# Kernel optimization log

Measured on AMD Instinct MI355X. Metric: run time of the kernel, lower is better.

## Reference

```python
import jax, jax.numpy as jnp
import numpy as np

B, S, D = 2, 2048, 1024
H, HKV, HD = 16, 4, 64
FF = 4096
WINDOW = 1024
EPS = 1e-6


def _rope_tables(seq_len, head_dim, base=10000.0):
    inv_freq = 1.0 / (base ** (np.arange(0, head_dim, 2, dtype=np.float32) / head_dim))
    t = np.arange(seq_len, dtype=np.float32)
    freqs = np.outer(t, inv_freq)                       # [S, HD/2]
    emb = np.concatenate([freqs, freqs], axis=-1)       # [S, HD]
    return jnp.asarray(np.cos(emb)), jnp.asarray(np.sin(emb))


def setup_inputs() -> dict:
    key = jax.random.key(0)
    ks = jax.random.split(key, 16)
    s = lambda fan: 1.0 / np.sqrt(fan)
    cos, sin = _rope_tables(S, HD)
    return {
        "hidden_states": jax.random.normal(ks[0], (B, S, D), jnp.float32),
        "cos": cos, "sin": sin,
        "wq": jax.random.normal(ks[1], (D, H * HD), jnp.float32) * s(D),
        "bq": jnp.zeros((H * HD,), jnp.float32),
        "wk": jax.random.normal(ks[2], (D, HKV * HD), jnp.float32) * s(D),
        "bk": jnp.zeros((HKV * HD,), jnp.float32),
        "wv": jax.random.normal(ks[3], (D, HKV * HD), jnp.float32) * s(D),
        "bv": jnp.zeros((HKV * HD,), jnp.float32),
        "wo": jax.random.normal(ks[4], (H * HD, D), jnp.float32) * s(H * HD),
        "ln1_w": jnp.ones((D,), jnp.float32),
        "ln2_w": jnp.ones((D,), jnp.float32),
        "w_gate": jax.random.normal(ks[5], (D, FF), jnp.float32) * s(D),
        "w_up": jax.random.normal(ks[6], (D, FF), jnp.float32) * s(D),
        "w_down": jax.random.normal(ks[7], (FF, D), jnp.float32) * s(FF),
    }


def _rmsnorm(x, w, eps=EPS):
    var = jnp.mean(x.astype(jnp.float32) ** 2, axis=-1, keepdims=True)
    return (x * jax.lax.rsqrt(var + eps)).astype(x.dtype) * w


def _rotate_half(x):
    x1, x2 = jnp.split(x, 2, axis=-1)
    return jnp.concatenate([-x2, x1], axis=-1)


def reference(hidden_states, cos, sin, wq, bq, wk, bk, wv, bv, wo,
              ln1_w, ln2_w, w_gate, w_up, w_down):
    residual = hidden_states
    h = _rmsnorm(hidden_states, ln1_w)

    # projections -> [B, S, H, HD]
    q = (h @ wq + bq).reshape(B, S, H, HD)
    k = (h @ wk + bk).reshape(B, S, HKV, HD)
    v = (h @ wv + bv).reshape(B, S, HKV, HD)

    # RoPE
    c = cos[None, :, None, :]
    sn = sin[None, :, None, :]
    q = q * c + _rotate_half(q) * sn
    k = k * c + _rotate_half(k) * sn

    # GQA: repeat KV heads to H heads
    groups = H // HKV
    k = jnp.repeat(k, groups, axis=2)  # [B, S, H, HD]
    v = jnp.repeat(v, groups, axis=2)

    # sliding-window causal attention (flex_attention block-mask semantics)
    scale = 1.0 / np.sqrt(HD)
    scores = jnp.einsum("bqhd,bkhd->bhqk", q, k) * scale  # [B, H, S, S]
    i = jnp.arange(S)[:, None]
    j = jnp.arange(S)[None, :]
    mask = (j <= i) & (i - j < WINDOW)
    scores = jnp.where(mask[None, None], scores, jnp.finfo(scores.dtype).min)
    attn = jax.nn.softmax(scores, axis=-1)
    ctx = jnp.einsum("bhqk,bkhd->bqhd", attn, v).reshape(B, S, H * HD)

    h = residual + ctx @ wo

    residual2 = h
    h2 = _rmsnorm(h, ln2_w)
    mlp = (jax.nn.silu(h2 @ w_gate) * (h2 @ w_up)) @ w_down
    return residual2 + mlp
```

## Files before the change

kernel.cpp:

```cpp
#include <hip/hip_runtime.h>
#include <hip/hip_bf16.h>
#include <hip/hip_fp16.h>
#include <math.h>

#define BB 2
#define SS 2048
#define DD 1024
#define HH 16
#define HKVN 4
#define HDIM 64
#define FFD 4096
#define WND 1024
#define EPSF 1e-6f

typedef _Float16 f16;
typedef _Float16 half8 __attribute__((ext_vector_type(8)));
typedef float f32x4 __attribute__((ext_vector_type(4)));
typedef unsigned int u32;

#define GLOAD_LDS(gp, lp)                                                  \
  __builtin_amdgcn_global_load_lds(                                        \
      (const __attribute__((address_space(1))) u32*)(gp),                  \
      (__attribute__((address_space(3))) u32*)(lp), 16, 0, 0)

static __device__ inline u32 pack2(float a, float b) {
  unsigned short ua = __builtin_bit_cast(unsigned short, (f16)a);
  unsigned short ub = __builtin_bit_cast(unsigned short, (f16)b);
  return (u32)ua | ((u32)ub << 16);
}

__global__ __launch_bounds__(256) void prep_weights_kernel(
    const float* __restrict__ wq, const float* __restrict__ wk,
    const float* __restrict__ wv, const float* __restrict__ wo,
    const float* __restrict__ wg, const float* __restrict__ wu,
    const float* __restrict__ wd, const float* __restrict__ bq,
    const float* __restrict__ bk, const float* __restrict__ bv,
    f16* __restrict__ qkvT, f16* __restrict__ woT, f16* __restrict__ wgT,
    f16* __restrict__ wuT, f16* __restrict__ wdT, float* __restrict__ biasC) {
  int t = blockIdx.x;
  if (t >= 3712) {
    int i = (t - 3712) * 256 + threadIdx.x;
    if (i < 1024)
      biasC[i] = bq[i];
    else if (i < 1280)
      biasC[i] = bk[i - 1024];
    else if (i < 1536)
      biasC[i] = bv[i - 1280];
    return;
  }
  const float* W;
  f16* Wt;
  int K, N, lt;
  if (t < 256) {
    W = wq; Wt = qkvT; K = 1024; N = 1024; lt = t;
  } else if (t < 320) {
    W = wk; Wt = qkvT + (size_t)1024 * 1024; K = 1024; N = 256; lt = t - 256;
  } else if (t < 384) {
    W = wv; Wt = qkvT + (size_t)1280 * 1024; K = 1024; N = 256; lt = t - 320;
  } else if (t < 640) {
    W = wo; Wt = woT; K = 1024; N = 1024; lt = t - 384;
  } else if (t < 1664) {
    W = wg; Wt = wgT; K = 1024; N = 4096; lt = t - 640;
  } else if (t < 2688) {
    W = wu; Wt = wuT; K = 1024; N = 4096; lt = t - 1664;
  } else {
    W = wd; Wt = wdT; K = 4096; N = 1024; lt = t - 2688;
  }
  int ntx = N >> 6;
  int n0 = (lt % ntx) * 64, k0 = (lt / ntx) * 64;
  __shared__ float tile[64][65];
  int tx = threadIdx.x & 63, tr = threadIdx.x >> 6;
#pragma unroll
  for (int i = 0; i < 16; i++) {
    int r = tr + i * 4;
    tile[r][tx] = W[(size_t)(k0 + r) * N + n0 + tx];
  }
  __syncthreads();
#pragma unroll
  for (int i = 0; i < 16; i++) {
    int r = tr + i * 4;
    Wt[(size_t)(n0 + r) * K + k0 + tx] = (f16)tile[tx][r];
  }
}

__global__ __launch_bounds__(256) void rmsnorm_kernel(
    const float* __restrict__ x, const float* __restrict__ w,
    f16* __restrict__ out) {
  int row = blockIdx.x;
  int tid = threadIdx.x;
  float4 v = ((const float4*)(x + (size_t)row * 1024))[tid];
  float ss = v.x * v.x + v.y * v.y + v.z * v.z + v.w * v.w;
  for (int o = 32; o > 0; o >>= 1) ss += __shfl_down(ss, o, 64);
  __shared__ float red[4];
  int wid = tid >> 6, lane = tid & 63;
  if (lane == 0) red[wid] = ss;
  __syncthreads();
  if (tid == 0)
    red[0] = rsqrtf((red[0] + red[1] + red[2] + red[3]) / 1024.f + EPSF);
  __syncthreads();
  float rs = red[0];
  float4 wv = ((const float4*)w)[tid];
  u32 lo = pack2(v.x * rs * wv.x, v.y * rs * wv.y);
  u32 hi = pack2(v.z * rs * wv.z, v.w * rs * wv.w);
  *(int2*)(out + (size_t)row * 1024 + tid * 4) = make_int2((int)lo, (int)hi);
}

__global__ __launch_bounds__(256) void mfma_gemm(
    const f16* __restrict__ A, const f16* __restrict__ Bt,
    const float* __restrict__ bias, const float* __restrict__ resid,
    float* __restrict__ Cf, float* __restrict__ Cf2, f16* __restrict__ Ch,
    int M, int N, int K, int KL) {
  __shared__ __align__(16) char smem[3 * 16384];
  const int tid = threadIdx.x;
  const int lane = tid & 63;
  const int wid = tid >> 6;
  const int wr = wid >> 1, wc = wid & 1;
  const int row0 = blockIdx.y * 128, col0 = blockIdx.x * 128;
  const int koff = blockIdx.z * KL;

  f32x4 acc[4][4];
#pragma unroll
  for (int m = 0; m < 4; m++)
#pragma unroll
    for (int n = 0; n < 4; n++) acc[m][n] = (f32x4){0.f, 0.f, 0.f, 0.f};

  auto stage = [&](int buf, int k0) {
    char* base = smem + buf * 16384;
#pragma unroll
    for (int q = 0; q < 2; q++) {
      int s = wid * 128 + q * 64 + lane;
      int r = s >> 2;
      int cg = (s & 3) ^ ((r >> 1) & 3);
      size_t goff = (size_t)r * K + k0 + cg * 8;
      u32 ldsb = (u32)((wid * 2 + q) * 1024);
      GLOAD_LDS(A + (size_t)row0 * K + goff, base + ldsb);
      GLOAD_LDS(Bt + (size_t)col0 * K + goff, base + 8192 + ldsb);
    }
  };
  auto off = [&](int r, int g) -> int {
    return r * 64 + ((g ^ ((r >> 1) & 3)) << 4);
  };

  const int nt = KL / 32;
  stage(0, koff);
  if (nt > 1) stage(1, koff + 32);
  int cur = 0;
  const int g = lane >> 4, l15 = lane & 15;
  for (int t = 0; t < nt; t++) {
    if (t + 1 < nt)
      asm volatile("s_waitcnt vmcnt(4)" ::: "memory");
    else
      asm volatile("s_waitcnt vmcnt(0)" ::: "memory");
    asm volatile("s_waitcnt lgkmcnt(0)" ::: "memory");
    __builtin_amdgcn_sched_barrier(0);
    __builtin_amdgcn_s_barrier();
    __builtin_amdgcn_sched_barrier(0);
    const char* base = smem + cur * 16384;
    half8 af[4], bf[4];
#pragma unroll
    for (int m = 0; m < 4; m++) {
      int r = wr * 64 + m * 16 + l15;
      af[m] = *(const half8*)(base + off(r, g));
    }
#pragma unroll
    for (int n = 0; n < 4; n++) {
      int c = wc * 64 + n * 16 + l15;
      bf[n] = *(const half8*)(base + 8192 + off(c, g));
    }
    if (t + 2 < nt) {
      int nb = cur + 2;
      if (nb >= 3) nb -= 3;
      stage(nb, koff + (t + 2) * 32);
    }
    __builtin_amdgcn_s_setprio(1);
#pragma unroll
    for (int m = 0; m < 4; m++)
#pragma unroll
      for (int n = 0; n < 4; n++)
        acc[m][n] =
            __builtin_amdgcn_mfma_f32_16x16x32_f16(af[m], bf[n], acc[m][n], 0, 0, 0);
    __builtin_amdgcn_s_setprio(0);
    cur = (cur + 1 == 3) ? 0 : cur + 1;
  }

  float* cw = (blockIdx.z == 0) ? Cf : Cf2;
#pragma unroll
  for (int m = 0; m < 4; m++) {
#pragma unroll
    for (int n = 0; n < 4; n++) {
#pragma unroll
      for (int v = 0; v < 4; v++) {
        int r = row0 + wr * 64 + m * 16 + (lane >> 4) * 4 + v;
        int c = col0 + wc * 64 + n * 16 + l15;
        float vv = acc[m][n][v];
        if (bias) vv += bias[c];
        if (Ch) {
          Ch[(size_t)r * N + c] = (f16)vv;
        } else {
          if (resid) vv += resid[(size_t)r * N + c];
          cw[(size_t)r * N + c] = vv;
        }
      }
    }
  }
}

__global__ __launch_bounds__(512) void gateup_gemm(
    const f16* __restrict__ A, const f16* __restrict__ Wg,
    const f16* __restrict__ Wu, f16* __restrict__ ACT, int M, int N, int K) {
  __shared__ __align__(16) char smem[3 * 40960];
  const int tid = threadIdx.x;
  const int lane = tid & 63;
  const int wid = tid >> 6;
  const int wr = wid >> 2;
  const int wc = wid & 3;
  const int row0 = blockIdx.y * 128, col0 = blockIdx.x * 256;

  f32x4 accg[4][4], accu[4][4];
#pragma unroll
  for (int m = 0; m < 4; m++)
#pragma unroll
    for (int n = 0; n < 4; n++) {
      accg[m][n] = (f32x4){0.f, 0.f, 0.f, 0.f};
      accu[m][n] = (f32x4){0.f, 0.f, 0.f, 0.f};
    }

  auto stage = [&](int buf, int k0) {
    char* base = smem + buf * 40960;
    {
      int s = tid;
      int r = s >> 2;
      int cg = (s & 3) ^ ((r >> 1) & 3);
      size_t goff = (size_t)r * K + k0 + cg * 8;
      GLOAD_LDS(A + (size_t)row0 * K + goff, base + wid * 1024);
    }
#pragma unroll
    for (int p = 0; p < 2; p++) {
      int s = p * 512 + tid;
      int r = s >> 2;
      int cg = (s & 3) ^ ((r >> 1) & 3);
      size_t goff = (size_t)r * K + k0 + cg * 8;
      GLOAD_LDS(Wg + (size_t)col0 * K + goff,
                base + 8192 + p * 8192 + wid * 1024);
    }
#pragma unroll
    for (int p = 0; p < 2; p++) {
      int s = p * 512 + tid;
      int r = s >> 2;
      int cg = (s & 3) ^ ((r >> 1) & 3);
      size_t goff = (size_t)r * K + k0 + cg * 8;
      GLOAD_LDS(Wu + (size_t)col0 * K + goff,
                base + 24576 + p * 8192 + wid * 1024);
    }
  };
  auto off = [&](int r, int g) -> int {
    return r * 64 + ((g ^ ((r >> 1) & 3)) << 4);
  };

  const int nt = K / 32;
  stage(0, 0);
  if (nt > 1) stage(1, 32);
  int cur = 0;
  const int g = lane >> 4, l15 = lane & 15;
  for (int t = 0; t < nt; t++) {
    if (t + 1 < nt)
      asm volatile("s_waitcnt vmcnt(5)" ::: "memory");
    else
      asm volatile("s_waitcnt vmcnt(0)" ::: "memory");
    asm volatile("s_waitcnt lgkmcnt(0)" ::: "memory");
    __builtin_amdgcn_sched_barrier(0);
    __builtin_amdgcn_s_barrier();
    __builtin_amdgcn_sched_barrier(0);
    const char* base = smem + cur * 40960;
    half8 af[4], gf[4], uf[4];
#pragma unroll
    for (int m = 0; m < 4; m++) {
      int r = wr * 64 + m * 16 + l15;
      af[m] = *(const half8*)(base + off(r, g));
    }
#pragma unroll
    for (int n = 0; n < 4; n++) {
      int c = wc * 64 + n * 16 + l15;
      gf[n] = *(const half8*)(base + 8192 + off(c, g));
      uf[n] = *(const half8*)(base + 24576 + off(c, g));
    }
    if (t + 2 < nt) {
      int nb = cur + 2;
      if (nb >= 3) nb -= 3;
      stage(nb, (t + 2) * 32);
    }
    __builtin_amdgcn_s_setprio(1);
#pragma unroll
    for (int m = 0; m < 4; m++)
#pragma unroll
      for (int n = 0; n < 4; n++) {
        accg[m][n] =
            __builtin_amdgcn_mfma_f32_16x16x32_f16(af[m], gf[n], accg[m][n], 0, 0, 0);
        accu[m][n] =
            __builtin_amdgcn_mfma_f32_16x16x32_f16(af[m], uf[n], accu[m][n], 0, 0, 0);
      }
    __builtin_amdgcn_s_setprio(0);
    cur = (cur + 1 == 3) ? 0 : cur + 1;
  }

#pragma unroll
  for (int m = 0; m < 4; m++) {
#pragma unroll
    for (int n = 0; n < 4; n++) {
#pragma unroll
      for (int v = 0; v < 4; v++) {
        int r = row0 + wr * 64 + m * 16 + (lane >> 4) * 4 + v;
        int c = col0 + wc * 64 + n * 16 + l15;
        float gg = accg[m][n][v];
        float uu = accu[m][n][v];
        float sv = gg / (1.f + __expf(-gg));
        ACT[(size_t)r * N + c] = (f16)(sv * uu);
      }
    }
  }
}

__global__ __launch_bounds__(256) void addreduce_kernel(
    const float* __restrict__ P0, const float* __restrict__ P1,
    float* __restrict__ out, int n4) {
  int idx = blockIdx.x * 256 + threadIdx.x;
  for (int i = idx; i < n4; i += gridDim.x * 256) {
    float4 a = ((const float4*)P0)[i];
    float4 b = ((const float4*)P1)[i];
    float4 o = ((float4*)out)[i];
    o.x += a.x + b.x;
    o.y += a.y + b.y;
    o.z += a.z + b.z;
    o.w += a.w + b.w;
    ((float4*)out)[i] = o;
  }
}

__global__ __launch_bounds__(256) void rope_cast_kernel(
    const f16* __restrict__ QKV, const float* __restrict__ cos_t,
    const float* __restrict__ sin_t, f16* __restrict__ Qh,
    f16* __restrict__ Kh) {
  int idx = blockIdx.x * blockDim.x + threadIdx.x;
  int d = idx & 31;
  int rest = idx >> 5;
  int head = rest % (HH + HKVN);
  int bs = rest / (HH + HKVN);
  int s = bs % SS;
  float c = cos_t[s * HDIM + d];
  float sn = sin_t[s * HDIM + d];
  const f16* rowp = QKV + (size_t)bs * 1536;
  if (head < HH) {
    const f16* base = rowp + head * HDIM;
    float x1 = (float)base[d], x2 = (float)base[d + 32];
    f16* ob = Qh + ((size_t)bs * HH + head) * HDIM;
    ob[d] = (f16)((x1 * c - x2 * sn) * 0.125f);
    ob[d + 32] = (f16)((x2 * c + x1 * sn) * 0.125f);
  } else {
    int hk = head - HH;
    const f16* base = rowp + 1024 + hk * HDIM;
    float x1 = (float)base[d], x2 = (float)base[d + 32];
    f16* ob = Kh + ((size_t)bs * HKVN + hk) * HDIM;
    ob[d] = (f16)(x1 * c - x2 * sn);
    ob[d + 32] = (f16)(x2 * c + x1 * sn);
  }
}

__global__ __launch_bounds__(256) void vtrans_kernel(
    const f16* __restrict__ QKV, f16* __restrict__ Vt) {
  __shared__ f16 tile[64][72];
  int st = blockIdx.x & 31;
  int hk = (blockIdx.x >> 5) & 3;
  int b = blockIdx.x >> 7;
  int s0 = st * 64;
  int tid = threadIdx.x;
  int r = tid >> 2, cg = tid & 3;
#pragma unroll
  for (int i = 0; i < 2; i++) {
    const f16* src = QKV + (size_t)(b * SS + s0 + r) * 1536 + 1280 + hk * HDIM +
                     cg * 16 + i * 8;
    *(int4*)&tile[r][cg * 16 + i * 8] = *(const int4*)src;
  }
  __syncthreads();
  int dd = tid >> 2, sg = tid & 3;
#pragma unroll
  for (int i = 0; i < 4; i++) {
    int c0 = sg * 16 + i * 4;
    unsigned short a0 = __builtin_bit_cast(unsigned short, tile[c0 + 0][dd]);
    unsigned short a1 = __builtin_bit_cast(unsigned short, tile[c0 + 1][dd]);
    unsigned short a2 = __builtin_bit_cast(unsigned short, tile[c0 + 2][dd]);
    unsigned short a3 = __builtin_bit_cast(unsigned short, tile[c0 + 3][dd]);
    u32 w0 = (u32)a0 | ((u32)a1 << 16);
    u32 w1 = (u32)a2 | ((u32)a3 << 16);
    *(int2*)(Vt + ((size_t)(b * HKVN + hk) * HDIM + dd) * SS + s0 + c0) =
        make_int2((int)w0, (int)w1);
  }
}

__global__ __launch_bounds__(256) void attn_kernel(
    const f16* __restrict__ Qh, const f16* __restrict__ Kh,
    const f16* __restrict__ Vt, f16* __restrict__ O) {
  __shared__ __align__(16) char smem[2 * 16384 + 4 * 4608];
  const int tid = threadIdx.x;
  const int lane = tid & 63;
  const int wid = tid >> 6;
  const int l15 = lane & 15;
  const int g = lane >> 4;
  int qt = blockIdx.x & 63;
  int hk = (blockIdx.x >> 6) & 3;
  int b = blockIdx.x >> 8;
  int s0 = qt * 32;
  int h = hk * 4 + wid;

  half8 qf[2][2];
#pragma unroll
  for (int n = 0; n < 2; n++) {
    int q = s0 + n * 16 + l15;
    const f16* qp = Qh + (((size_t)b * SS + q) * HH + h) * HDIM;
#pragma unroll
    for (int kk = 0; kk < 2; kk++) qf[n][kk] = *(const half8*)(qp + kk * 32 + g * 8);
  }

  const int tb = (s0 >= WND) ? ((s0 - (WND - 1)) >> 6) : 0;
  const int te = (s0 + 31) >> 6;

  f32x4 acc_o[2][4];
#pragma unroll
  for (int m2 = 0; m2 < 2; m2++)
#pragma unroll
    for (int n = 0; n < 4; n++) acc_o[m2][n] = (f32x4){0.f, 0.f, 0.f, 0.f};
  float mrun[2] = {-1e30f, -1e30f};
  float lrun[2] = {0.f, 0.f};

  char* pw = smem + 32768 + wid * 4608;

  auto stage = [&](int buf, int tt) {
    int jt0 = tt * 64;
    char* kbase = smem + buf * 16384;
#pragma unroll
    for (int q2 = 0; q2 < 2; q2++) {
      int slot = (wid * 2 + q2) * 64 + lane;
      int r = slot >> 3, c = slot & 7;
      int cc = c ^ (r & 7);
      u32 ldsb = (u32)((wid * 2 + q2) * 1024);
      const f16* gk =
          Kh + ((size_t)(b * SS + jt0 + r) * HKVN + hk) * HDIM + cc * 8;
      GLOAD_LDS(gk, kbase + ldsb);
      const f16* gv =
          Vt + ((size_t)(b * HKVN + hk) * HDIM + r) * SS + jt0 + cc * 8;
      GLOAD_LDS(gv, kbase + 8192 + ldsb);
    }
  };

  stage(0, tb);
  __syncthreads();
  for (int tt = tb; tt <= te; tt++) {
    int buf = (tt - tb) & 1;
    if (tt < te) stage(buf ^ 1, tt + 1);
    const char* kb = smem + buf * 16384;
    const char* vbp = kb + 8192;
    int jt0 = tt * 64;

    f32x4 acc_s[4][2];
#pragma unroll
    for (int m = 0; m < 4; m++)
#pragma unroll
      for (int n = 0; n < 2; n++) acc_s[m][n] = (f32x4){0.f, 0.f, 0.f, 0.f};
#pragma unroll
    for (int kk = 0; kk < 2; kk++) {
      half8 af[4];
#pragma unroll
      for (int m = 0; m < 4; m++) {
        int key = m * 16 + l15;
        af[m] = *(const half8*)(kb + key * 128 + (((kk * 4 + g) ^ (key & 7)) << 4));
      }
#pragma unroll
      for (int m = 0; m < 4; m++)
#pragma unroll
        for (int n = 0; n < 2; n++)
          acc_s[m][n] = __builtin_amdgcn_mfma_f32_16x16x32_f16(af[m], qf[n][kk],
                                                               acc_s[m][n], 0, 0, 0);
    }

    float tmax[2] = {-1e38f, -1e38f};
#pragma unroll
    for (int m = 0; m < 4; m++)
#pragma unroll
      for (int n = 0; n < 2; n++)
#pragma unroll
        for (int v = 0; v < 4; v++) {
          int j = jt0 + m * 16 + g * 4 + v;
          int q = s0 + n * 16 + l15;
          float s = acc_s[m][n][v];
          s = ((unsigned)(q - j) < (unsigned)WND) ? s : -1e38f;
          acc_s[m][n][v] = s;
          tmax[n] = fmaxf(tmax[n], s);
        }
#pragma unroll
    for (int n = 0; n < 2; n++) {
      tmax[n] = fmaxf(tmax[n], __shfl_xor(tmax[n], 16, 64));
      tmax[n] = fmaxf(tmax[n], __shfl_xor(tmax[n], 32, 64));
    }
    float corr[2], rs[2];
#pragma unroll
    for (int n = 0; n < 2; n++) {
      float mn = fmaxf(mrun[n], tmax[n]);
      corr[n] = __expf(mrun[n] - mn);
      mrun[n] = mn;
      rs[n] = 0.f;
    }
#pragma unroll
    for (int m = 0; m < 4; m++)
#pragma unroll
      for (int n = 0; n < 2; n++) {
        float p0 = __expf(acc_s[m][n][0] - mrun[n]);
        float p1 = __expf(acc_s[m][n][1] - mrun[n]);
        float p2 = __expf(acc_s[m][n][2] - mrun[n]);
        float p3 = __expf(acc_s[m][n][3] - mrun[n]);
        rs[n] += (p0 + p1) + (p2 + p3);
        *(int2*)(pw + (n * 16 + l15) * 144 + (m * 16 + g * 4) * 2) =
            make_int2((int)pack2(p0, p1), (int)pack2(p2, p3));
      }
#pragma unroll
    for (int n = 0; n < 2; n++) {
      rs[n] += __shfl_xor(rs[n], 16, 64);
      rs[n] += __shfl_xor(rs[n], 32, 64);
      lrun[n] = lrun[n] * corr[n] + rs[n];
    }
#pragma unroll
    for (int m2 = 0; m2 < 2; m2++)
#pragma unroll
      for (int v = 0; v < 4; v++) {
        float cw = __shfl(corr[m2], g * 4 + v, 64);
#pragma unroll
        for (int n = 0; n < 4; n++) acc_o[m2][n][v] *= cw;
      }
#pragma unroll
    for (int kk = 0; kk < 2; kk++) {
      half8 ap[2], vf[4];
#pragma unroll
      for (int m2 = 0; m2 < 2; m2++)
        ap[m2] = *(const half8*)(pw + (m2 * 16 + l15) * 144 + (kk * 32 + g * 8) * 2);
#pragma unroll
      for (int n = 0; n < 4; n++) {
        int d = n * 16 + l15;
        vf[n] = *(const half8*)(vbp + d * 128 + (((kk * 4 + g) ^ (d & 7)) << 4));
      }
#pragma unroll
      for (int m2 = 0; m2 < 2; m2++)
#pragma unroll
        for (int n = 0; n < 4; n++)
          acc_o[m2][n] = __builtin_amdgcn_mfma_f32_16x16x32_f16(ap[m2], vf[n],
                                                                acc_o[m2][n], 0, 0, 0);
    }
    __syncthreads();
  }

#pragma unroll
  for (int m2 = 0; m2 < 2; m2++)
#pragma unroll
    for (int v = 0; v < 4; v++) {
      float li = __shfl(lrun[m2], g * 4 + v, 64);
      float inv = 1.f / li;
      int q = s0 + m2 * 16 + g * 4 + v;
#pragma unroll
      for (int n = 0; n < 4; n++) {
        int d = n * 16 + l15;
        O[(((size_t)b * SS + q) * HH + h) * HDIM + d] =
            (f16)(acc_o[m2][n][v] * inv);
      }
    }
}

extern "C" void kernel_launch(void* const* d_in, const int* in_sizes, int n_in,
                              void* d_out, int out_size, void* d_ws,
                              size_t ws_size, hipStream_t stream) {
  const float* hidden = (const float*)d_in[0];
  const float* cos_t = (const float*)d_in[1];
  const float* sin_t = (const float*)d_in[2];
  const float* wq = (const float*)d_in[3];
  const float* bq = (const float*)d_in[4];
  const float* wk = (const float*)d_in[5];
  const float* bk = (const float*)d_in[6];
  const float* wv = (const float*)d_in[7];
  const float* bv = (const float*)d_in[8];
  const float* wo = (const float*)d_in[9];
  const float* ln1 = (const float*)d_in[10];
  const float* ln2 = (const float*)d_in[11];
  const float* wg = (const float*)d_in[12];
  const float* wu = (const float*)d_in[13];
  const float* wd = (const float*)d_in[14];
  float* out = (float*)d_out;
  char* ws = (char*)d_ws;

  const int M = BB * SS;

  f16* qkvT = (f16*)ws;
  f16* woT = (f16*)(ws + (3u << 20));
  f16* wgT = (f16*)(ws + (5u << 20));
  f16* wuT = (f16*)(ws + (13u << 20));
  f16* wdT = (f16*)(ws + (21u << 20));
  f16* Anh = (f16*)(ws + (29u << 20));
  f16* CTXh = (f16*)(ws + (37u << 20));
  f16* QKVh = (f16*)(ws + (45u << 20));
  f16* Qh = (f16*)(ws + (57u << 20));
  f16* Kh = (f16*)(ws + (65u << 20));
  f16* Vt = (f16*)(ws + (67u << 20));
  f16* ACTh = (f16*)(ws + (45u << 20));
  float* P0 = (float*)(ws + (29u << 20));
  float* P1 = (float*)(ws + (5u << 20));
  float* biasC = (float*)(ws + (81u << 20));

  prep_weights_kernel<<<3718, 256, 0, stream>>>(wq, wk, wv, wo, wg, wu, wd, bq,
                                                bk, bv, qkvT, woT, wgT, wuT,
                                                wdT, biasC);
  rmsnorm_kernel<<<M, 256, 0, stream>>>(hidden, ln1, Anh);
  mfma_gemm<<<dim3(1536 / 128, M / 128, 1), 256, 0, stream>>>(
      Anh, qkvT, biasC, nullptr, nullptr, nullptr, QKVh, M, 1536, DD, DD);
  rope_cast_kernel<<<(BB * SS * (HH + HKVN) * 32) / 256, 256, 0, stream>>>(
      QKVh, cos_t, sin_t, Qh, Kh);
  vtrans_kernel<<<BB * HKVN * (SS / 64), 256, 0, stream>>>(QKVh, Vt);
  attn_kernel<<<BB * HKVN * (SS / 32), 256, 0, stream>>>(Qh, Kh, Vt, CTXh);
  mfma_gemm<<<dim3(DD / 128, M / 128, 1), 256, 0, stream>>>(
      CTXh, woT, nullptr, hidden, out, nullptr, nullptr, M, DD, DD, DD);
  rmsnorm_kernel<<<M, 256, 0, stream>>>(out, ln2, Anh);
  gateup_gemm<<<dim3(FFD / 256, M / 128), 512, 0, stream>>>(Anh, wgT, wuT, ACTh,
                                                            M, FFD, DD);
  mfma_gemm<<<dim3(DD / 128, M / 128, 2), 256, 0, stream>>>(
      ACTh, wdT, nullptr, nullptr, P0, P1, nullptr, M, DD, FFD, FFD / 2);
  addreduce_kernel<<<2048, 256, 0, stream>>>(P0, P1, out, M * DD / 4);
}
```

Measured before the change: 274.8 us.

## Drop split-K down projection and fuse residual add; pack transpose stores

```diff
diff --git a/kernel.cpp b/kernel.cpp
--- a/kernel.cpp
+++ b/kernel.cpp
@@ -76,10 +76,13 @@
     tile[r][tx] = W[(size_t)(k0 + r) * N + n0 + tx];
   }
   __syncthreads();
-#pragma unroll
-  for (int i = 0; i < 16; i++) {
-    int r = tr + i * 4;
-    Wt[(size_t)(n0 + r) * K + k0 + tx] = (f16)tile[tx][r];
+  int kx = (threadIdx.x & 31) * 2;
+  int rr = threadIdx.x >> 5;
+#pragma unroll
+  for (int i = 0; i < 8; i++) {
+    int r = rr + i * 8;
+    u32 w = pack2(tile[kx][r], tile[kx + 1][r]);
+    *(u32*)(Wt + (size_t)(n0 + r) * K + k0 + kx) = w;
   }
 }
 
@@ -108,15 +111,13 @@
 __global__ __launch_bounds__(256) void mfma_gemm(
     const f16* __restrict__ A, const f16* __restrict__ Bt,
     const float* __restrict__ bias, const float* __restrict__ resid,
-    float* __restrict__ Cf, float* __restrict__ Cf2, f16* __restrict__ Ch,
-    int M, int N, int K, int KL) {
+    float* __restrict__ Cf, f16* __restrict__ Ch, int M, int N, int K) {
   __shared__ __align__(16) char smem[3 * 16384];
   const int tid = threadIdx.x;
   const int lane = tid & 63;
   const int wid = tid >> 6;
   const int wr = wid >> 1, wc = wid & 1;
   const int row0 = blockIdx.y * 128, col0 = blockIdx.x * 128;
-  const int koff = blockIdx.z * KL;
 
   f32x4 acc[4][4];
 #pragma unroll
@@ -141,9 +142,9 @@
     return r * 64 + ((g ^ ((r >> 1) & 3)) << 4);
   };
 
-  const int nt = KL / 32;
-  stage(0, koff);
-  if (nt > 1) stage(1, koff + 32);
+  const int nt = K / 32;
+  stage(0, 0);
+  if (nt > 1) stage(1, 32);
   int cur = 0;
   const int g = lane >> 4, l15 = lane & 15;
   for (int t = 0; t < nt; t++) {
@@ -170,7 +171,7 @@
     if (t + 2 < nt) {
       int nb = cur + 2;
       if (nb >= 3) nb -= 3;
-      stage(nb, koff + (t + 2) * 32);
+      stage(nb, (t + 2) * 32);
     }
     __builtin_amdgcn_s_setprio(1);
 #pragma unroll
@@ -183,7 +184,6 @@
     cur = (cur + 1 == 3) ? 0 : cur + 1;
   }
 
-  float* cw = (blockIdx.z == 0) ? Cf : Cf2;
 #pragma unroll
   for (int m = 0; m < 4; m++) {
 #pragma unroll
@@ -198,7 +198,7 @@
           Ch[(size_t)r * N + c] = (f16)vv;
         } else {
           if (resid) vv += resid[(size_t)r * N + c];
-          cw[(size_t)r * N + c] = vv;
+          Cf[(size_t)r * N + c] = vv;
         }
       }
     }
@@ -317,22 +317,6 @@
         ACT[(size_t)r * N + c] = (f16)(sv * uu);
       }
     }
-  }
-}
-
-__global__ __launch_bounds__(256) void addreduce_kernel(
-    const float* __restrict__ P0, const float* __restrict__ P1,
-    float* __restrict__ out, int n4) {
-  int idx = blockIdx.x * 256 + threadIdx.x;
-  for (int i = idx; i < n4; i += gridDim.x * 256) {
-    float4 a = ((const float4*)P0)[i];
-    float4 b = ((const float4*)P1)[i];
-    float4 o = ((float4*)out)[i];
-    o.x += a.x + b.x;
-    o.y += a.y + b.y;
-    o.z += a.z + b.z;
-    o.w += a.w + b.w;
-    ((float4*)out)[i] = o;
   }
 }
 
@@ -606,26 +590,23 @@
   f16* Kh = (f16*)(ws + (65u << 20));
   f16* Vt = (f16*)(ws + (67u << 20));
   f16* ACTh = (f16*)(ws + (45u << 20));
-  float* P0 = (float*)(ws + (29u << 20));
-  float* P1 = (float*)(ws + (5u << 20));
   float* biasC = (float*)(ws + (81u << 20));
 
   prep_weights_kernel<<<3718, 256, 0, stream>>>(wq, wk, wv, wo, wg, wu, wd, bq,
                                                 bk, bv, qkvT, woT, wgT, wuT,
                                                 wdT, biasC);
   rmsnorm_kernel<<<M, 256, 0, stream>>>(hidden, ln1, Anh);
-  mfma_gemm<<<dim3(1536 / 128, M / 128, 1), 256, 0, stream>>>(
-      Anh, qkvT, biasC, nullptr, nullptr, nullptr, QKVh, M, 1536, DD, DD);
+  mfma_gemm<<<dim3(1536 / 128, M / 128), 256, 0, stream>>>(
+      Anh, qkvT, biasC, nullptr, nullptr, QKVh, M, 1536, DD);
   rope_cast_kernel<<<(BB * SS * (HH + HKVN) * 32) / 256, 256, 0, stream>>>(
       QKVh, cos_t, sin_t, Qh, Kh);
   vtrans_kernel<<<BB * HKVN * (SS / 64), 256, 0, stream>>>(QKVh, Vt);
   attn_kernel<<<BB * HKVN * (SS / 32), 256, 0, stream>>>(Qh, Kh, Vt, CTXh);
-  mfma_gemm<<<dim3(DD / 128, M / 128, 1), 256, 0, stream>>>(
-      CTXh, woT, nullptr, hidden, out, nullptr, nullptr, M, DD, DD, DD);
+  mfma_gemm<<<dim3(DD / 128, M / 128), 256, 0, stream>>>(
+      CTXh, woT, nullptr, hidden, out, nullptr, M, DD, DD);
   rmsnorm_kernel<<<M, 256, 0, stream>>>(out, ln2, Anh);
   gateup_gemm<<<dim3(FFD / 256, M / 128), 512, 0, stream>>>(Anh, wgT, wuT, ACTh,
                                                             M, FFD, DD);
-  mfma_gemm<<<dim3(DD / 128, M / 128, 2), 256, 0, stream>>>(
-      ACTh, wdT, nullptr, nullptr, P0, P1, nullptr, M, DD, FFD, FFD / 2);
-  addreduce_kernel<<<2048, 256, 0, stream>>>(P0, P1, out, M * DD / 4);
-}
+  mfma_gemm<<<dim3(DD / 128, M / 128), 256, 0, stream>>>(
+      ACTh, wdT, nullptr, out, out, nullptr, M, DD, FFD);
+}
```

Measured after the change: 276.4 us. Within noise of the previous version (+0.6%).
